# Performance work log

Hardware: AMD Instinct MI355X
Metric: run time of the kernel (lower is better)

Reference implementation:

```python
import jax, jax.numpy as jnp
import numpy as np

G, N_AST = 8192, 32
D_EMB, H_IN, ENC, H_OUT = 128, 64, 128, 128
N_STMT, E_STMT, N_SEL = G, 32768, 4096
EPS, NEG = 1e-5, 0.2


def _bn(x, g, b):
    # PyG BatchNorm (BatchNorm1d over nodes), training-mode batch stats (biased var)
    mu = x.mean(0)
    var = ((x - mu) ** 2).mean(0)
    return (x - mu) * jax.lax.rsqrt(var + EPS) * g + b


def _seg_softmax(logits, seg, n):
    # numerically stable softmax over edges grouped by destination node
    m = jax.ops.segment_max(logits, seg, num_segments=n)
    m = jnp.where(jnp.isfinite(m), m, 0.0)
    e = jnp.exp(logits - m[seg])
    s = jax.ops.segment_sum(e, seg, num_segments=n)
    return e / jnp.maximum(s[seg], 1e-16)


def _gat(x, src, dst, emask, W, a_src, a_dst, bias, heads, C, n):
    # PyG GATConv: add self-loops, leaky_relu(0.2) attention, concat heads, + bias
    h = (x @ W).reshape(n, heads, C)
    asrc = (h * a_src).sum(-1)  # [n, H]
    adst = (h * a_dst).sum(-1)
    loops = jnp.arange(n, dtype=src.dtype)
    s = jnp.concatenate([src, loops])
    d = jnp.concatenate([dst, loops])
    m = jnp.concatenate([emask, jnp.ones(n, bool)])
    logits = jax.nn.leaky_relu(asrc[s] + adst[d], NEG)
    logits = jnp.where(m[:, None], logits, -1e9)
    alpha = _seg_softmax(logits, d, n)  # [E, H]
    msg = jnp.where(m[:, None, None], alpha[:, :, None] * h[s], 0.0)
    out = jax.ops.segment_sum(msg, d, num_segments=n)
    return out.reshape(n, heads * C) + bias


def _topk(x, src, dst, emask, w, n_per_g, ratio, num_g):
    # PyG TopKPooling: score = tanh(x.w/||w||), keep top ceil(ratio*n) per graph,
    # gate kept features by score, remap/filter edges (here: mask + remap).
    k = int(np.ceil(ratio * n_per_g))
    score = (x @ w) / jnp.linalg.norm(w)  # [num_g*n_per_g]
    top_sc, top_idx = jax.lax.top_k(score.reshape(num_g, n_per_g), k)
    perm = (top_idx + jnp.arange(num_g)[:, None] * n_per_g).reshape(-1)
    new_x = x[perm] * jnp.tanh(top_sc).reshape(-1, 1)
    new_id = jnp.full((num_g * n_per_g,), -1, jnp.int32).at[perm].set(
        jnp.arange(num_g * k, dtype=jnp.int32))
    ns, nd = new_id[src], new_id[dst]
    valid = emask & (ns >= 0) & (nd >= 0)
    return new_x, jnp.maximum(ns, 0), jnp.maximum(nd, 0), valid, k


def _rgat(x, src, dst, etype, W, q, katt, bias, heads, C, n):
    # PyG RGATConv: per-relation weight, additive self-attention, across-relation softmax
    h0, h1 = x @ W[0], x @ W[1]  # [n, H*C]
    rel = (etype == 1)[:, None]
    out_j = jnp.where(rel, h1[src], h0[src])
    out_i = jnp.where(rel, h1[dst], h0[dst])
    logits = jax.nn.leaky_relu(out_i @ q + out_j @ katt, NEG)  # [E, H]
    alpha = _seg_softmax(logits, dst, n)
    msg = alpha[:, :, None] * out_j.reshape(-1, heads, C)
    out = jax.ops.segment_sum(msg, dst, num_segments=n)
    return out.reshape(n, heads * C) + bias


def setup_inputs() -> dict:
    key = jax.random.key(0)
    ks = jax.random.split(key, 20)
    rng = np.random.default_rng(0)
    # AST forest: random tree per statement graph (parent -> child edges)
    parents = np.stack([rng.integers(0, i, size=G) for i in range(1, N_AST)], axis=1)
    offs = (np.arange(G) * N_AST)[:, None]
    ast_src = jnp.asarray((parents + offs).reshape(-1), jnp.int32)
    ast_dst = jnp.asarray((np.broadcast_to(np.arange(1, N_AST), (G, N_AST - 1)) + offs).reshape(-1), jnp.int32)
    # statement-level graph; edge_type sorted (relation 0 block then relation 1)
    stmt_src = jnp.asarray(rng.integers(0, N_STMT, E_STMT), jnp.int32)
    stmt_dst = jnp.asarray(rng.integers(0, N_STMT, E_STMT), jnp.int32)
    stmt_etype = jnp.asarray(np.sort(rng.integers(0, 2, E_STMT)), jnp.int32)
    sel_index = jnp.asarray(np.sort(rng.choice(N_STMT, N_SEL, replace=False)), jnp.int32)

    def nrm(k, shape, s=0.1):
        return jax.random.normal(k, shape, jnp.float32) * s

    return dict(
        ast_x=jax.random.normal(ks[0], (G * N_AST, D_EMB), jnp.float32),
        ast_src=ast_src, ast_dst=ast_dst,
        stmt_src=stmt_src, stmt_dst=stmt_dst, stmt_etype=stmt_etype,
        sel_index=sel_index,
        gat0_W=nrm(ks[1], (D_EMB, 3 * H_IN)),
        gat0_asrc=nrm(ks[2], (3, H_IN)), gat0_adst=nrm(ks[3], (3, H_IN)),
        gat0_b=jnp.zeros((3 * H_IN,), jnp.float32),
        bn0_g=jnp.ones((3 * H_IN,), jnp.float32), bn0_b=jnp.zeros((3 * H_IN,), jnp.float32),
        pool0_w=nrm(ks[4], (3 * H_IN,)),
        gat1_W=nrm(ks[5], (3 * H_IN, H_IN)),
        gat1_asrc=nrm(ks[6], (1, H_IN)), gat1_adst=nrm(ks[7], (1, H_IN)),
        gat1_b=jnp.zeros((H_IN,), jnp.float32),
        bn1_g=jnp.ones((H_IN,), jnp.float32), bn1_b=jnp.zeros((H_IN,), jnp.float32),
        pool1_w=nrm(ks[8], (H_IN,)),
        enc_w1=nrm(ks[9], (H_IN, H_IN)), enc_b1=jnp.zeros((H_IN,), jnp.float32),
        enc_w2=nrm(ks[10], (H_IN, ENC)), enc_b2=jnp.zeros((ENC,), jnp.float32),
        rgat0_W=nrm(ks[11], (2, ENC, 3 * H_OUT)),
        rgat0_q=nrm(ks[12], (3 * H_OUT, 3)), rgat0_k=nrm(ks[13], (3 * H_OUT, 3)),
        rgat0_b=jnp.zeros((3 * H_OUT,), jnp.float32),
        bnc0_g=jnp.ones((3 * H_OUT,), jnp.float32), bnc0_b=jnp.zeros((3 * H_OUT,), jnp.float32),
        rgat1_W=nrm(ks[14], (2, 3 * H_OUT, H_OUT)),
        rgat1_q=nrm(ks[15], (H_OUT, 1)), rgat1_k=nrm(ks[16], (H_OUT, 1)),
        rgat1_b=jnp.zeros((H_OUT,), jnp.float32),
        bnc1_g=jnp.ones((H_OUT,), jnp.float32), bnc1_b=jnp.zeros((H_OUT,), jnp.float32),
        clf_w1=nrm(ks[17], (H_OUT, H_OUT)), clf_b1=jnp.zeros((H_OUT,), jnp.float32),
        clf_w2=nrm(ks[18], (H_OUT, 1)), clf_b2=jnp.zeros((1,), jnp.float32),
    )


def reference(ast_x, ast_src, ast_dst, stmt_src, stmt_dst, stmt_etype, sel_index,
              gat0_W, gat0_asrc, gat0_adst, gat0_b, bn0_g, bn0_b, pool0_w,
              gat1_W, gat1_asrc, gat1_adst, gat1_b, bn1_g, bn1_b, pool1_w,
              enc_w1, enc_b1, enc_w2, enc_b2,
              rgat0_W, rgat0_q, rgat0_k, rgat0_b, bnc0_g, bnc0_b,
              rgat1_W, rgat1_q, rgat1_k, rgat1_b, bnc1_g, bnc1_b,
              clf_w1, clf_b1, clf_w2, clf_b2):
    # ---- StatementEncoder over batch of AST graphs ----
    N0 = G * N_AST
    m_full = jnp.ones(ast_src.shape[0], bool)
    h = _gat(ast_x, ast_src, ast_dst, m_full, gat0_W, gat0_asrc, gat0_adst, gat0_b, 3, H_IN, N0)
    h = _bn(jnp.tanh(h), bn0_g, bn0_b)
    h, s, d, m, k0 = _topk(h, ast_src, ast_dst, m_full, pool0_w, N_AST, 0.7, G)
    h = jax.nn.relu(h)
    h = _gat(h, s, d, m, gat1_W, gat1_asrc, gat1_adst, gat1_b, 1, H_IN, G * k0)
    h = _bn(jnp.tanh(h), bn1_g, bn1_b)
    h, s, d, m, k1 = _topk(h, s, d, m, pool1_w, k0, 0.5, G)
    h = jax.nn.relu(h.reshape(G, k1, H_IN).max(axis=1))  # global_max_pool then relu
    x = jax.nn.relu(h @ enc_w1 + enc_b1) @ enc_w2 + enc_b2  # [G, ENC]
    # ---- StatementClassifier over statement graph ----
    h = _rgat(x, stmt_src, stmt_dst, stmt_etype, rgat0_W, rgat0_q, rgat0_k, rgat0_b, 3, H_OUT, N_STMT)
    h = _bn(jnp.tanh(h), bnc0_g, bnc0_b)
    h = _rgat(h, stmt_src, stmt_dst, stmt_etype, rgat1_W, rgat1_q, rgat1_k, rgat1_b, 1, H_OUT, N_STMT)
    h = _bn(jnp.tanh(h), bnc1_g, bnc1_b)
    h = h[sel_index]  # index_select(idx2index(idx))
    return jax.nn.sigmoid(jax.nn.relu(h @ clf_w1 + clf_b1) @ clf_w2 + clf_b2)
```

## Files before the change

kernel.cpp:

```cpp
#include <hip/hip_runtime.h>
#include <cstddef>
#include <cstdint>

constexpr int G      = 8192;
constexpr int NAST   = 32;
constexpr int N0     = G * NAST;
constexpr int D_EMB  = 128;
constexpr int C0     = 192;
constexpr int H_IN   = 64;
constexpr int K0     = 23;
constexpr int N1     = G * K0;
constexpr int K1     = 12;
constexpr int ENC    = 128;
constexpr int NSTMT  = 8192;
constexpr int EST    = 32768;
constexpr int HO3    = 384;
constexpr int HOUT   = 128;
constexpr int NSEL   = 4096;

__global__ __launch_bounds__(256) void fused_gat0(
    const float* __restrict__ X, const float* __restrict__ W,
    const int* __restrict__ ast_src,
    const float* __restrict__ asrc_w, const float* __restrict__ adst_w,
    const float* __restrict__ bias,
    float* __restrict__ out, float* __restrict__ psum, float* __restrict__ psq)
{
    __shared__ char smem[52736];
    int tid = threadIdx.x;
    int b = blockIdx.x;
    int row0 = b * 64;

    float* As = (float*)smem;
    float* Bs = As + 32 * 65;

    int ra = tid >> 3;
    int c0 = (tid & 7) * 24;
    int lr = tid >> 2;
    int lk = (tid & 3) * 8;
    int bkk = tid >> 3;
    int bc0 = (tid & 7) * 24;

    float acc0[24] = {};
    float acc1[24] = {};

    for (int kt = 0; kt < 128; kt += 32) {
        const float* ap = X + (size_t)(row0 + lr) * 128 + kt + lk;
        float4 a0 = *(const float4*)ap;
        float4 a1 = *(const float4*)(ap + 4);
        As[(lk + 0) * 65 + lr] = a0.x; As[(lk + 1) * 65 + lr] = a0.y;
        As[(lk + 2) * 65 + lr] = a0.z; As[(lk + 3) * 65 + lr] = a0.w;
        As[(lk + 4) * 65 + lr] = a1.x; As[(lk + 5) * 65 + lr] = a1.y;
        As[(lk + 6) * 65 + lr] = a1.z; As[(lk + 7) * 65 + lr] = a1.w;
        const float* bp = W + (size_t)(kt + bkk) * 192 + bc0;
        #pragma unroll
        for (int u = 0; u < 6; ++u)
            *(float4*)&Bs[bkk * 200 + bc0 + u * 4] = *(const float4*)(bp + u * 4);
        __syncthreads();
        #pragma unroll
        for (int kk = 0; kk < 32; ++kk) {
            float a0v = As[kk * 65 + ra];
            float a1v = As[kk * 65 + 32 + ra];
            const float* bb = &Bs[kk * 200 + c0];
            #pragma unroll
            for (int u = 0; u < 6; ++u) {
                float4 b4 = *(const float4*)(bb + u * 4);
                acc0[u * 4 + 0] += a0v * b4.x; acc1[u * 4 + 0] += a1v * b4.x;
                acc0[u * 4 + 1] += a0v * b4.y; acc1[u * 4 + 1] += a1v * b4.y;
                acc0[u * 4 + 2] += a0v * b4.z; acc1[u * 4 + 2] += a1v * b4.z;
                acc0[u * 4 + 3] += a0v * b4.w; acc1[u * 4 + 3] += a1v * b4.w;
            }
        }
        __syncthreads();
    }

    float* Cs  = (float*)smem;
    float* as_ = Cs + 64 * 193;
    float* ad_ = as_ + 192;
    float* aS  = ad_ + 192;
    float* aP  = aS + 192;
    int*  parl = (int*)(aP + 192);

    #pragma unroll
    for (int u = 0; u < 24; ++u) {
        Cs[ra * 193 + c0 + u]        = acc0[u];
        Cs[(ra + 32) * 193 + c0 + u] = acc1[u];
    }
    if (tid < 62) {
        int q = tid / 31, j = tid % 31 + 1;
        int g = 2 * b + q;
        parl[q * 32 + j] = ast_src[(size_t)g * 31 + j - 1] - g * 32 + q * 32;
    }
    if (tid < 2) parl[tid * 32] = -1;
    __syncthreads();

    for (int task = tid; task < 384; task += 256) {
        int r = task / 6, q6 = task % 6, hh = q6 >> 1, sd = q6 & 1;
        const float* w = (sd ? adst_w : asrc_w) + hh * 64;
        const float* crow = &Cs[r * 193 + hh * 64];
        float s = 0.f;
        for (int c = 0; c < 64; ++c) s += crow[c] * w[c];
        (sd ? ad_ : as_)[r * 3 + hh] = s;
    }
    __syncthreads();
    if (tid < 192) {
        int r = tid / 3, hh = tid % 3, p = parl[r];
        if (p < 0) { aS[r * 3 + hh] = 1.f; aP[r * 3 + hh] = 0.f; }
        else {
            float ls = as_[r * 3 + hh] + ad_[r * 3 + hh]; ls = ls > 0 ? ls : 0.2f * ls;
            float lp = as_[p * 3 + hh] + ad_[r * 3 + hh]; lp = lp > 0 ? lp : 0.2f * lp;
            float m = fmaxf(ls, lp);
            float es = __expf(ls - m) , ep = __expf(lp - m);
            es = expf(ls - m); ep = expf(lp - m);
            float inv = 1.f / (es + ep);
            aS[r * 3 + hh] = es * inv; aP[r * 3 + hh] = ep * inv;
        }
    }
    __syncthreads();
    if (tid < 192) {
        int j = tid, hh = j >> 6;
        float bj = bias[j];
        float s = 0.f, s2 = 0.f;
        for (int r = 0; r < 64; ++r) {
            int p = parl[r];
            float v = aS[r * 3 + hh] * Cs[r * 193 + j];
            if (p >= 0) v += aP[r * 3 + hh] * Cs[p * 193 + j];
            v = tanhf(v + bj);
            out[(size_t)(row0 + r) * 192 + j] = v;
            s += v; s2 += v * v;
        }
        psum[(size_t)j * 4096 + b] = s;
        psq [(size_t)j * 4096 + b] = s2;
    }
}

__global__ __launch_bounds__(256) void bn_finalize(
    const float* __restrict__ psum, const float* __restrict__ psq, int nb, float R,
    const float* __restrict__ gamma, const float* __restrict__ beta,
    const float* __restrict__ w,
    float* __restrict__ ga, float* __restrict__ be,
    float* __restrict__ gw, float* __restrict__ bw)
{
    int j = blockIdx.x, t = threadIdx.x;
    const float* ps = psum + (size_t)j * nb;
    const float* pq = psq + (size_t)j * nb;
    float s = 0.f, s2 = 0.f;
    for (int i = t; i < nb; i += 256) { s += ps[i]; s2 += pq[i]; }
    __shared__ float r1[4], r2[4];
    for (int o = 32; o > 0; o >>= 1) { s += __shfl_down(s, o, 64); s2 += __shfl_down(s2, o, 64); }
    if ((t & 63) == 0) { r1[t >> 6] = s; r2[t >> 6] = s2; }
    __syncthreads();
    if (t == 0) {
        float S = r1[0] + r1[1] + r1[2] + r1[3];
        float S2 = r2[0] + r2[1] + r2[2] + r2[3];
        float mu = S / R, var = S2 / R - mu * mu;
        float inv = 1.f / sqrtf(var + 1e-5f);
        float gaj = gamma[j] * inv, bej = beta[j] - mu * gaj;
        ga[j] = gaj; be[j] = bej; gw[j] = gaj * w[j]; bw[j] = bej * w[j];
    }
}

__global__ __launch_bounds__(256) void score_topk0(
    const float* __restrict__ hA, const int* __restrict__ ast_src,
    const float* __restrict__ gw, const float* __restrict__ bw,
    const float* __restrict__ w,
    int* __restrict__ oldrow, float* __restrict__ gate23, int* __restrict__ parloc)
{
    __shared__ float swv[192];
    __shared__ float sc[32];
    __shared__ int nid[32];
    __shared__ float wparts[4], bparts[4];
    int g = blockIdx.x, t = threadIdx.x;
    if (t < 192) swv[t] = gw[t];
    float ws = (t < 192) ? w[t] * w[t] : 0.f;
    float bs = (t < 192) ? bw[t] : 0.f;
    for (int o = 32; o > 0; o >>= 1) { ws += __shfl_down(ws, o, 64); bs += __shfl_down(bs, o, 64); }
    if ((t & 63) == 0) { wparts[t >> 6] = ws; bparts[t >> 6] = bs; }
    __syncthreads();
    float invn = rsqrtf(wparts[0] + wparts[1] + wparts[2] + wparts[3]);
    invn = 1.f / sqrtf(1.f / (invn * invn));
    {
        float tot = wparts[0] + wparts[1] + wparts[2] + wparts[3];
        invn = 1.f / sqrtf(tot);
    }
    float sb = bparts[0] + bparts[1] + bparts[2] + bparts[3];

    int r = t >> 3, j0 = (t & 7) * 24;
    const float* row = hA + ((size_t)g * 32 + r) * 192 + j0;
    const float4* row4 = (const float4*)row;
    const float4* sw4 = (const float4*)(swv + j0);
    float s = 0.f;
    #pragma unroll
    for (int u = 0; u < 6; ++u) {
        float4 a = row4[u], bv = sw4[u];
        s += a.x * bv.x + a.y * bv.y + a.z * bv.z + a.w * bv.w;
    }
    for (int o = 4; o > 0; o >>= 1) s += __shfl_down(s, o, 8);
    if ((t & 7) == 0) sc[r] = (s + sb) * invn;
    __syncthreads();
    if (t < 32) {
        float v = sc[t]; int rank = 0;
        for (int j = 0; j < 32; ++j) rank += (sc[j] > v) || (sc[j] == v && j < t);
        nid[t] = (rank < 23) ? rank : -1;
    }
    __syncthreads();
    if (t < 32 && nid[t] >= 0) {
        int rank = nid[t];
        oldrow[g * 23 + rank] = g * 32 + t;
        gate23[g * 23 + rank] = tanhf(sc[t]);
        int pl = -1;
        if (t > 0) {
            int p = ast_src[(size_t)g * 31 + t - 1] - g * 32;
            pl = nid[p];
        }
        parloc[g * 23 + rank] = pl;
    }
}

__global__ __launch_bounds__(256) void gemm_gather(
    const float* __restrict__ A, const float* __restrict__ B, float* __restrict__ C,
    const int* __restrict__ rowmap, const float* __restrict__ gate,
    const float* __restrict__ ga, const float* __restrict__ be)
{
    __shared__ float As[16 * 68];
    __shared__ float Bs[16 * 68];
    __shared__ float gas[192], bes[192];
    int tid = threadIdx.x, bm = blockIdx.x;
    if (tid < 192) { gas[tid] = ga[tid]; bes[tid] = be[tid]; }
    int arow = tid >> 2, aks = (tid & 3) * 4;
    int brow = tid >> 4, bns = (tid & 15) * 4;
    int tm = tid >> 4, tn = tid & 15;
    float acc[4][4] = {};
    int grow = bm * 64 + arow;
    int old = rowmap[grow];
    float gt = gate[grow];
    const float* ap = A + (size_t)old * 192;
    __syncthreads();
    for (int kt = 0; kt < 192; kt += 16) {
        float4 av = *(const float4*)(ap + kt + aks);
        int kb = kt + aks;
        av.x = fmaxf((av.x * gas[kb + 0] + bes[kb + 0]) * gt, 0.f);
        av.y = fmaxf((av.y * gas[kb + 1] + bes[kb + 1]) * gt, 0.f);
        av.z = fmaxf((av.z * gas[kb + 2] + bes[kb + 2]) * gt, 0.f);
        av.w = fmaxf((av.w * gas[kb + 3] + bes[kb + 3]) * gt, 0.f);
        As[(aks + 0) * 68 + arow] = av.x;
        As[(aks + 1) * 68 + arow] = av.y;
        As[(aks + 2) * 68 + arow] = av.z;
        As[(aks + 3) * 68 + arow] = av.w;
        *(float4*)&Bs[brow * 68 + bns] = *(const float4*)(B + (size_t)(kt + brow) * 64 + bns);
        __syncthreads();
        #pragma unroll
        for (int kk = 0; kk < 16; ++kk) {
            float4 a4 = *(const float4*)&As[kk * 68 + (tm << 2)];
            float4 b4 = *(const float4*)&Bs[kk * 68 + (tn << 2)];
            float a_[4] = {a4.x, a4.y, a4.z, a4.w};
            float b_[4] = {b4.x, b4.y, b4.z, b4.w};
            #pragma unroll
            for (int i = 0; i < 4; ++i)
                #pragma unroll
                for (int j = 0; j < 4; ++j)
                    acc[i][j] += a_[i] * b_[j];
        }
        __syncthreads();
    }
    #pragma unroll
    for (int i = 0; i < 4; ++i) {
        int rr = bm * 64 + (tm << 2) + i;
        float4 o = {acc[i][0], acc[i][1], acc[i][2], acc[i][3]};
        *(float4*)(C + (size_t)rr * 64 + (tn << 2)) = o;
    }
}

__global__ __launch_bounds__(64) void gat1_att_bn(
    float* __restrict__ h, const int* __restrict__ parloc,
    const float* __restrict__ aw_s, const float* __restrict__ aw_d,
    const float* __restrict__ bias,
    float* __restrict__ psum, float* __restrict__ psq)
{
    __shared__ float hs[23 * 65];
    __shared__ float as_[23], ad_[23], aS[23], aP[23];
    __shared__ int parl[23];
    int g = blockIdx.x, t = threadIdx.x;
    float* base = h + (size_t)g * 23 * 64;
    for (int r = 0; r < 23; ++r) hs[r * 65 + t] = base[r * 64 + t];
    if (t < 23) parl[t] = parloc[g * 23 + t];
    __syncthreads();
    if (t < 46) {
        int r = t >> 1, sd = t & 1;
        const float* w = sd ? aw_d : aw_s;
        const float* row = &hs[r * 65];
        float s = 0.f;
        for (int c = 0; c < 64; ++c) s += row[c] * w[c];
        (sd ? ad_ : as_)[r] = s;
    }
    __syncthreads();
    if (t < 23) {
        int p = parl[t];
        if (p < 0) { aS[t] = 1.f; aP[t] = 0.f; }
        else {
            float ls = as_[t] + ad_[t]; ls = ls > 0 ? ls : 0.2f * ls;
            float lp = as_[p] + ad_[t]; lp = lp > 0 ? lp : 0.2f * lp;
            float m = fmaxf(ls, lp);
            float es = expf(ls - m), ep = expf(lp - m);
            float inv = 1.f / (es + ep);
            aS[t] = es * inv; aP[t] = ep * inv;
        }
    }
    __syncthreads();
    float bj = bias[t], s = 0.f, s2 = 0.f;
    for (int r = 0; r < 23; ++r) {
        int p = parl[r];
        float v = aS[r] * hs[r * 65 + t];
        if (p >= 0) v += aP[r] * hs[p * 65 + t];
        v = tanhf(v + bj);
        base[r * 64 + t] = v;
        s += v; s2 += v * v;
    }
    psum[(size_t)t * 8192 + g] = s;
    psq [(size_t)t * 8192 + g] = s2;
}

__global__ __launch_bounds__(128) void pool1_mlp(
    const float* __restrict__ h,
    const float* __restrict__ gw, const float* __restrict__ bw,
    const float* __restrict__ w,
    const float* __restrict__ ga, const float* __restrict__ be,
    const float* __restrict__ w1, const float* __restrict__ b1,
    const float* __restrict__ w2, const float* __restrict__ b2,
    float* __restrict__ xenc)
{
    __shared__ float hs[23 * 65];
    __shared__ float sc[23];
    __shared__ int keep[23];
    __shared__ float feat[64], t1[64];
    __shared__ float consts[2];
    int g = blockIdx.x, t = threadIdx.x;
    const float* base = h + (size_t)g * 23 * 64;
    {
        int c = t & 63;
        for (int r = t >> 6; r < 23; r += 2) hs[r * 65 + c] = base[r * 64 + c];
    }
    if (t < 64) {
        float ws = w[t] * w[t], bs = bw[t];
        for (int o = 32; o > 0; o >>= 1) { ws += __shfl_down(ws, o, 64); bs += __shfl_down(bs, o, 64); }
        if (t == 0) { consts[0] = 1.f / sqrtf(ws); consts[1] = bs; }
    }
    __syncthreads();
    if (t < 23) {
        const float* row = &hs[t * 65];
        float s = 0.f;
        for (int c = 0; c < 64; ++c) s += row[c] * gw[c];
        sc[t] = (s + consts[1]) * consts[0];
    }
    __syncthreads();
    if (t < 23) {
        float v = sc[t]; int rank = 0;
        for (int j = 0; j < 23; ++j) rank += (sc[j] > v) || (sc[j] == v && j < t);
        keep[t] = rank < 12;
    }
    __syncthreads();
    if (t < 23) sc[t] = tanhf(sc[t]);
    __syncthreads();
    if (t < 64) {
        float m = -1e30f, gac = ga[t], bec = be[t];
        for (int r = 0; r < 23; ++r)
            if (keep[r]) m = fmaxf(m, (hs[r * 65 + t] * gac + bec) * sc[r]);
        feat[t] = fmaxf(m, 0.f);
    }
    __syncthreads();
    if (t < 64) {
        float acc = b1[t];
        for (int c = 0; c < 64; ++c) acc += feat[c] * w1[c * 64 + t];
        t1[t] = fmaxf(acc, 0.f);
    }
    __syncthreads();
    float acc = b2[t];
    for (int j = 0; j < 64; ++j) acc += t1[j] * w2[j * 128 + t];
    xenc[(size_t)g * 128 + t] = acc;
}

__global__ __launch_bounds__(256) void gemm_nn(
    const float* __restrict__ A, const float* __restrict__ B, float* __restrict__ C,
    int M, int N, int K)
{
    __shared__ float As[16 * 68];
    __shared__ float Bs[16 * 68];
    int tid = threadIdx.x;
    int bm = blockIdx.x, bn = blockIdx.y;
    int arow = tid >> 2, aks = (tid & 3) * 4;
    int brow = tid >> 4, bns = (tid & 15) * 4;
    int tm = tid >> 4, tn = tid & 15;
    float acc[4][4] = {};
    const float* ap = A + (size_t)(bm * 64 + arow) * K;
    for (int kt = 0; kt < K; kt += 16) {
        float4 av = *(const float4*)(ap + kt + aks);
        As[(aks + 0) * 68 + arow] = av.x;
        As[(aks + 1) * 68 + arow] = av.y;
        As[(aks + 2) * 68 + arow] = av.z;
        As[(aks + 3) * 68 + arow] = av.w;
        *(float4*)&Bs[brow * 68 + bns] = *(const float4*)(B + (size_t)(kt + brow) * N + bn * 64 + bns);
        __syncthreads();
        #pragma unroll
        for (int kk = 0; kk < 16; ++kk) {
            float4 a4 = *(const float4*)&As[kk * 68 + (tm << 2)];
            float4 b4 = *(const float4*)&Bs[kk * 68 + (tn << 2)];
            float a_[4] = {a4.x, a4.y, a4.z, a4.w};
            float b_[4] = {b4.x, b4.y, b4.z, b4.w};
            #pragma unroll
            for (int i = 0; i < 4; ++i)
                #pragma unroll
                for (int j = 0; j < 4; ++j)
                    acc[i][j] += a_[i] * b_[j];
        }
        __syncthreads();
    }
    #pragma unroll
    for (int i = 0; i < 4; ++i) {
        int r = bm * 64 + (tm << 2) + i;
        float4 o = {acc[i][0], acc[i][1], acc[i][2], acc[i][3]};
        *(float4*)(C + (size_t)r * N + bn * 64 + (tn << 2)) = o;
    }
}

__global__ void bn_stats(const float* __restrict__ X, int R,
                         float* __restrict__ sum, float* __restrict__ sumsq)
{
    int t = threadIdx.x;
    int C = blockDim.x;
    float s = 0.f, s2 = 0.f;
    for (int r = blockIdx.x; r < R; r += gridDim.x) {
        float v = X[(size_t)r * C + t];
        s += v; s2 += v * v;
    }
    atomicAdd(&sum[t], s);
    atomicAdd(&sumsq[t], s2);
}

__global__ void bn_apply(float* __restrict__ X, int R,
                         const float* __restrict__ sum, const float* __restrict__ sumsq,
                         const float* __restrict__ gam, const float* __restrict__ bet)
{
    int t = threadIdx.x;
    int C = blockDim.x;
    float invR = 1.f / (float)R;
    float mu = sum[t] * invR;
    float var = sumsq[t] * invR - mu * mu;
    float inv = 1.f / sqrtf(var + 1e-5f);
    float ga = gam[t] * inv;
    float be = bet[t] - mu * ga;
    for (int r = blockIdx.x; r < R; r += gridDim.x) {
        size_t idx = (size_t)r * C + t;
        X[idx] = X[idx] * ga + be;
    }
}

__global__ __launch_bounds__(256) void rgat_qk3(
    const float* __restrict__ h0, const float* __restrict__ h1,
    const float* __restrict__ q, const float* __restrict__ k,
    float* __restrict__ qi, float* __restrict__ kj)
{
    int n = blockIdx.x, t = threadIdx.x;
    float p[12] = {};
    for (int d = t; d < HO3; d += 256) {
        float v0 = h0[(size_t)n * HO3 + d], v1 = h1[(size_t)n * HO3 + d];
        #pragma unroll
        for (int hh = 0; hh < 3; ++hh) {
            float qw = q[d * 3 + hh], kw = k[d * 3 + hh];
            p[hh]     += v0 * qw;  p[3 + hh] += v0 * kw;
            p[6 + hh] += v1 * qw;  p[9 + hh] += v1 * kw;
        }
    }
    __shared__ float red[4][12];
    #pragma unroll
    for (int i = 0; i < 12; ++i) {
        float x = p[i];
        for (int o = 32; o > 0; o >>= 1) x += __shfl_down(x, o, 64);
        if ((t & 63) == 0) red[t >> 6][i] = x;
    }
    __syncthreads();
    if (t < 12) {
        float s = red[0][t] + red[1][t] + red[2][t] + red[3][t];
        int rel = t / 6, rem = t % 6, isk = rem / 3, hh = rem % 3;
        float* dst = isk ? kj : qi;
        dst[((size_t)rel * NSTMT + n) * 3 + hh] = s;
    }
}

__global__ void edge_logits3(const int* __restrict__ src, const int* __restrict__ dst,
                             const int* __restrict__ et,
                             const float* __restrict__ qi, const float* __restrict__ kj,
                             float* __restrict__ logits)
{
    int e = blockIdx.x * 256 + threadIdx.x;
    if (e >= EST) return;
    int r = et[e], s = src[e], d = dst[e];
    #pragma unroll
    for (int hh = 0; hh < 3; ++hh) {
        float x = qi[((size_t)r * NSTMT + d) * 3 + hh] + kj[((size_t)r * NSTMT + s) * 3 + hh];
        logits[e * 3 + hh] = x > 0 ? x : 0.2f * x;
    }
}

__global__ void count_deg(const int* __restrict__ dst, int* __restrict__ deg)
{
    int e = blockIdx.x * 256 + threadIdx.x;
    if (e < EST) atomicAdd(&deg[dst[e]], 1);
}

__global__ void scan_deg(const int* __restrict__ deg, int* __restrict__ offa)
{
    __shared__ int ts[1024];
    int t = threadIdx.x;
    int base = t * 8;
    int loc[8]; int s = 0;
    #pragma unroll
    for (int i = 0; i < 8; ++i) { loc[i] = s; s += deg[base + i]; }
    ts[t] = s;
    __syncthreads();
    for (int o = 1; o < 1024; o <<= 1) {
        int v = (t >= o) ? ts[t - o] : 0;
        __syncthreads();
        ts[t] += v;
        __syncthreads();
    }
    int prev = (t == 0) ? 0 : ts[t - 1];
    #pragma unroll
    for (int i = 0; i < 8; ++i) offa[base + i] = prev + loc[i];
    if (t == 1023) offa[8192] = ts[1023];
}

__global__ void scatter_csr(const int* __restrict__ dst, const int* __restrict__ offa,
                            int* __restrict__ cnt, int* __restrict__ csr)
{
    int e = blockIdx.x * 256 + threadIdx.x;
    if (e < EST) {
        int d = dst[e];
        int pos = offa[d] + atomicAdd(&cnt[d], 1);
        csr[pos] = e;
    }
}

__global__ __launch_bounds__(256) void rgat_agg3(
    const float* __restrict__ h0, const float* __restrict__ h1,
    const int* __restrict__ offa, const int* __restrict__ csr,
    const int* __restrict__ src, const int* __restrict__ et,
    const float* __restrict__ logits, const float* __restrict__ bias,
    float* __restrict__ out)
{
    int n = blockIdx.x, t = threadIdx.x;
    int o0 = offa[n], deg = offa[n + 1] - o0;
    __shared__ float m[3], sden[3];
    __shared__ float al[64][3];
    __shared__ int esrc[64], erel[64];
    if (t < 3) {
        float mm = -1e30f;
        for (int i = 0; i < deg; ++i) mm = fmaxf(mm, logits[csr[o0 + i] * 3 + t]);
        float ss = 0.f;
        for (int i = 0; i < deg; ++i) ss += expf(logits[csr[o0 + i] * 3 + t] - mm);
        m[t] = mm; sden[t] = fmaxf(ss, 1e-16f);
    }
    __syncthreads();
    float acc0 = 0.f, acc1 = 0.f;
    for (int c0 = 0; c0 < deg; c0 += 64) {
        int cn = min(64, deg - c0);
        if (t < cn) { int e = csr[o0 + c0 + t]; esrc[t] = src[e]; erel[t] = et[e]; }
        if (t < cn * 3) {
            int ee = t / 3, hh = t % 3;
            int e = csr[o0 + c0 + ee];
            al[ee][hh] = expf(logits[e * 3 + hh] - m[hh]) / sden[hh];
        }
        __syncthreads();
        for (int i = 0; i < cn; ++i) {
            const float* hb = (erel[i] ? h1 : h0) + (size_t)esrc[i] * HO3;
            acc0 += al[i][t >> 7] * hb[t];
            if (t < 128) acc1 += al[i][(t + 256) >> 7] * hb[t + 256];
        }
        __syncthreads();
    }
    out[(size_t)n * HO3 + t] = tanhf(acc0 + bias[t]);
    if (t < 128) out[(size_t)n * HO3 + t + 256] = tanhf(acc1 + bias[t + 256]);
}

__global__ __launch_bounds__(128) void rgat_qk1(
    const float* __restrict__ h0, const float* __restrict__ h1,
    const float* __restrict__ q, const float* __restrict__ k,
    float* __restrict__ qi, float* __restrict__ kj)
{
    int n = blockIdx.x, t = threadIdx.x;
    float v0 = h0[(size_t)n * 128 + t], v1 = h1[(size_t)n * 128 + t];
    float p0 = v0 * q[t], p1 = v0 * k[t], p2 = v1 * q[t], p3 = v1 * k[t];
    __shared__ float red[2][4];
    for (int o = 32; o > 0; o >>= 1) {
        p0 += __shfl_down(p0, o, 64); p1 += __shfl_down(p1, o, 64);
        p2 += __shfl_down(p2, o, 64); p3 += __shfl_down(p3, o, 64);
    }
    if ((t & 63) == 0) { int w = t >> 6; red[w][0] = p0; red[w][1] = p1; red[w][2] = p2; red[w][3] = p3; }
    __syncthreads();
    if (t < 4) {
        float s = red[0][t] + red[1][t];
        if (t == 0) qi[n] = s;
        else if (t == 1) kj[n] = s;
        else if (t == 2) qi[NSTMT + n] = s;
        else kj[NSTMT + n] = s;
    }
}

__global__ void edge_logits1(const int* __restrict__ src, const int* __restrict__ dst,
                             const int* __restrict__ et,
                             const float* __restrict__ qi, const float* __restrict__ kj,
                             float* __restrict__ logits)
{
    int e = blockIdx.x * 256 + threadIdx.x;
    if (e >= EST) return;
    int r = et[e], s = src[e], d = dst[e];
    float x = qi[(size_t)r * NSTMT + d] + kj[(size_t)r * NSTMT + s];
    logits[e] = x > 0 ? x : 0.2f * x;
}

__global__ __launch_bounds__(128) void rgat_agg1(
    const float* __restrict__ h0, const float* __restrict__ h1,
    const int* __restrict__ offa, const int* __restrict__ csr,
    const int* __restrict__ src, const int* __restrict__ et,
    const float* __restrict__ logits, const float* __restrict__ bias,
    float* __restrict__ out)
{
    int n = blockIdx.x, t = threadIdx.x;
    int o0 = offa[n], deg = offa[n + 1] - o0;
    __shared__ float m1, s1;
    __shared__ float al[64];
    __shared__ int esrc[64], erel[64];
    if (t == 0) {
        float mm = -1e30f;
        for (int i = 0; i < deg; ++i) mm = fmaxf(mm, logits[csr[o0 + i]]);
        float ss = 0.f;
        for (int i = 0; i < deg; ++i) ss += expf(logits[csr[o0 + i]] - mm);
        m1 = mm; s1 = fmaxf(ss, 1e-16f);
    }
    __syncthreads();
    float acc = 0.f;
    for (int c0 = 0; c0 < deg; c0 += 64) {
        int cn = min(64, deg - c0);
        if (t < cn) {
            int e = csr[o0 + c0 + t];
            esrc[t] = src[e]; erel[t] = et[e];
            al[t] = expf(logits[e] - m1) / s1;
        }
        __syncthreads();
        for (int i = 0; i < cn; ++i)
            acc += al[i] * ((erel[i] ? h1 : h0)[(size_t)esrc[i] * 128 + t]);
        __syncthreads();
    }
    out[(size_t)n * 128 + t] = tanhf(acc + bias[t]);
}

__global__ __launch_bounds__(128) void classifier(
    const float* __restrict__ x, const int* __restrict__ sel,
    const float* __restrict__ w1, const float* __restrict__ b1,
    const float* __restrict__ w2, const float* __restrict__ b2,
    float* __restrict__ out)
{
    __shared__ float row[128];
    __shared__ float t1[128];
    __shared__ float red[2];
    int b = blockIdx.x, t = threadIdx.x;
    int n = sel[b];
    row[t] = x[(size_t)n * 128 + t];
    __syncthreads();
    float acc = b1[t];
    for (int k = 0; k < 128; ++k) acc += row[k] * w1[k * 128 + t];
    t1[t] = fmaxf(acc, 0.f);
    __syncthreads();
    float p = t1[t] * w2[t];
    for (int o = 32; o > 0; o >>= 1) p += __shfl_down(p, o, 64);
    if ((t & 63) == 0) red[t >> 6] = p;
    __syncthreads();
    if (t == 0) {
        float z = red[0] + red[1] + b2[0];
        out[b] = 1.f / (1.f + expf(-z));
    }
}

constexpr size_t OFF_HA     = 0;
constexpr size_t OFF_BN0    = 201326592;
constexpr size_t OFF_BN1    = OFF_BN0 + 3072;
constexpr size_t OFF_OLDROW = OFF_BN1 + 1024;
constexpr size_t OFF_GATE   = OFF_OLDROW + 753664;
constexpr size_t OFF_PARLOC = OFF_GATE + 753664;
constexpr size_t OFF_HB     = OFF_PARLOC + 753664;
constexpr size_t OFF_XENC   = OFF_HB + 48234496;
constexpr size_t OFF_BNSUM  = OFF_XENC + 4194304;
constexpr size_t OFF_BNSQ   = OFF_BNSUM + 1536;
constexpr size_t WS_NEEDED  = OFF_BNSQ + 1536;
constexpr size_t OFF_H0R  = 0;
constexpr size_t OFF_H1R  = 12582912;
constexpr size_t OFF_OUT0 = 25165824;
constexpr size_t OFF_G0   = 37748736;
constexpr size_t OFF_G1   = 41943040;
constexpr size_t OFF_OUT1 = 46137344;
constexpr size_t OFF_QI3  = 50331648;
constexpr size_t OFF_KJ3  = 50528256;
constexpr size_t OFF_LG3  = 50724864;
constexpr size_t OFF_QI1  = 51118080;
constexpr size_t OFF_KJ1  = 51183616;
constexpr size_t OFF_LG1  = 51249152;
constexpr size_t OFF_DEG  = 51380224;
constexpr size_t OFF_OFFA = 51412992;
constexpr size_t OFF_CNT  = 51446016;
constexpr size_t OFF_CSR  = 51478784;

extern "C" void kernel_launch(void* const* d_in, const int* in_sizes, int n_in,
                              void* d_out, int out_size, void* d_ws, size_t ws_size,
                              hipStream_t stream)
{
    if (n_in < 41 || ws_size < WS_NEEDED) return;

    const float* ast_x    = (const float*)d_in[0];
    const int*   ast_src  = (const int*)d_in[1];
    const int*   stmt_src = (const int*)d_in[3];
    const int*   stmt_dst = (const int*)d_in[4];
    const int*   stmt_et  = (const int*)d_in[5];
    const int*   sel      = (const int*)d_in[6];
    const float* gat0_W    = (const float*)d_in[7];
    const float* gat0_asrc = (const float*)d_in[8];
    const float* gat0_adst = (const float*)d_in[9];
    const float* gat0_b    = (const float*)d_in[10];
    const float* bn0_g     = (const float*)d_in[11];
    const float* bn0_b     = (const float*)d_in[12];
    const float* pool0_w   = (const float*)d_in[13];
    const float* gat1_W    = (const float*)d_in[14];
    const float* gat1_asrc = (const float*)d_in[15];
    const float* gat1_adst = (const float*)d_in[16];
    const float* gat1_b    = (const float*)d_in[17];
    const float* bn1_g     = (const float*)d_in[18];
    const float* bn1_b     = (const float*)d_in[19];
    const float* pool1_w   = (const float*)d_in[20];
    const float* enc_w1    = (const float*)d_in[21];
    const float* enc_b1    = (const float*)d_in[22];
    const float* enc_w2    = (const float*)d_in[23];
    const float* enc_b2    = (const float*)d_in[24];
    const float* rgat0_W   = (const float*)d_in[25];
    const float* rgat0_q   = (const float*)d_in[26];
    const float* rgat0_k   = (const float*)d_in[27];
    const float* rgat0_b   = (const float*)d_in[28];
    const float* bnc0_g    = (const float*)d_in[29];
    const float* bnc0_b    = (const float*)d_in[30];
    const float* rgat1_W   = (const float*)d_in[31];
    const float* rgat1_q   = (const float*)d_in[32];
    const float* rgat1_k   = (const float*)d_in[33];
    const float* rgat1_b   = (const float*)d_in[34];
    const float* bnc1_g    = (const float*)d_in[35];
    const float* bnc1_b    = (const float*)d_in[36];
    const float* clf_w1    = (const float*)d_in[37];
    const float* clf_b1    = (const float*)d_in[38];
    const float* clf_w2    = (const float*)d_in[39];
    const float* clf_b2    = (const float*)d_in[40];

    char* ws = (char*)d_ws;
    float* hA     = (float*)(ws + OFF_HA);
    float* ga0    = (float*)(ws + OFF_BN0);
    float* be0    = ga0 + 192;
    float* gw0    = be0 + 192;
    float* bw0    = gw0 + 192;
    float* ga1    = (float*)(ws + OFF_BN1);
    float* be1    = ga1 + 64;
    float* gw1    = be1 + 64;
    float* bw1    = gw1 + 64;
    int*   oldrow = (int*)(ws + OFF_OLDROW);
    float* gate23 = (float*)(ws + OFF_GATE);
    int*   parloc = (int*)(ws + OFF_PARLOC);
    float* hB     = (float*)(ws + OFF_HB);
    float* psum0  = (float*)(ws + OFF_HB);
    float* psq0   = psum0 + 192 * 4096;
    float* xenc   = (float*)(ws + OFF_XENC);
    float* psum1  = (float*)(ws + OFF_XENC);
    float* psq1   = psum1 + 64 * 8192;
    float* bnsum  = (float*)(ws + OFF_BNSUM);
    float* bnsq   = (float*)(ws + OFF_BNSQ);

    float* h0r  = (float*)(ws + OFF_H0R);
    float* h1r  = (float*)(ws + OFF_H1R);
    float* out0 = (float*)(ws + OFF_OUT0);
    float* g0   = (float*)(ws + OFF_G0);
    float* g1   = (float*)(ws + OFF_G1);
    float* out1 = (float*)(ws + OFF_OUT1);
    float* qi3  = (float*)(ws + OFF_QI3);
    float* kj3  = (float*)(ws + OFF_KJ3);
    float* lg3  = (float*)(ws + OFF_LG3);
    float* qi1  = (float*)(ws + OFF_QI1);
    float* kj1  = (float*)(ws + OFF_KJ1);
    float* lg1  = (float*)(ws + OFF_LG1);
    int*   deg  = (int*)(ws + OFF_DEG);
    int*   offa = (int*)(ws + OFF_OFFA);
    int*   cnt  = (int*)(ws + OFF_CNT);
    int*   csr  = (int*)(ws + OFF_CSR);

    fused_gat0<<<4096, 256, 0, stream>>>(ast_x, gat0_W, ast_src, gat0_asrc, gat0_adst,
                                         gat0_b, hA, psum0, psq0);
    bn_finalize<<<192, 256, 0, stream>>>(psum0, psq0, 4096, (float)N0,
                                         bn0_g, bn0_b, pool0_w, ga0, be0, gw0, bw0);
    score_topk0<<<G, 256, 0, stream>>>(hA, ast_src, gw0, bw0, pool0_w,
                                       oldrow, gate23, parloc);
    gemm_gather<<<N1 / 64, 256, 0, stream>>>(hA, gat1_W, hB, oldrow, gate23, ga0, be0);
    gat1_att_bn<<<G, 64, 0, stream>>>(hB, parloc, gat1_asrc, gat1_adst, gat1_b,
                                      psum1, psq1);
    bn_finalize<<<64, 256, 0, stream>>>(psum1, psq1, 8192, (float)N1,
                                        bn1_g, bn1_b, pool1_w, ga1, be1, gw1, bw1);
    pool1_mlp<<<G, 128, 0, stream>>>(hB, gw1, bw1, pool1_w, ga1, be1,
                                     enc_w1, enc_b1, enc_w2, enc_b2, xenc);

    gemm_nn<<<dim3(NSTMT / 64, HO3 / 64), 256, 0, stream>>>(xenc, rgat0_W, h0r, NSTMT, HO3, ENC);
    gemm_nn<<<dim3(NSTMT / 64, HO3 / 64), 256, 0, stream>>>(xenc, rgat0_W + (size_t)ENC * HO3, h1r, NSTMT, HO3, ENC);
    rgat_qk3<<<NSTMT, 256, 0, stream>>>(h0r, h1r, rgat0_q, rgat0_k, qi3, kj3);
    edge_logits3<<<EST / 256, 256, 0, stream>>>(stmt_src, stmt_dst, stmt_et, qi3, kj3, lg3);
    hipMemsetAsync(deg, 0, 32768, stream);
    hipMemsetAsync(cnt, 0, 32768, stream);
    count_deg<<<EST / 256, 256, 0, stream>>>(stmt_dst, deg);
    scan_deg<<<1, 1024, 0, stream>>>(deg, offa);
    scatter_csr<<<EST / 256, 256, 0, stream>>>(stmt_dst, offa, cnt, csr);
    rgat_agg3<<<NSTMT, 256, 0, stream>>>(h0r, h1r, offa, csr, stmt_src, stmt_et, lg3, rgat0_b, out0);
    hipMemsetAsync(bnsum, 0, 3072, stream);
    bn_stats<<<256, HO3, 0, stream>>>(out0, NSTMT, bnsum, bnsq);
    bn_apply<<<256, HO3, 0, stream>>>(out0, NSTMT, bnsum, bnsq, bnc0_g, bnc0_b);
    gemm_nn<<<dim3(NSTMT / 64, HOUT / 64), 256, 0, stream>>>(out0, rgat1_W, g0, NSTMT, HOUT, HO3);
    gemm_nn<<<dim3(NSTMT / 64, HOUT / 64), 256, 0, stream>>>(out0, rgat1_W + (size_t)HO3 * HOUT, g1, NSTMT, HOUT, HO3);
    rgat_qk1<<<NSTMT, 128, 0, stream>>>(g0, g1, rgat1_q, rgat1_k, qi1, kj1);
    edge_logits1<<<EST / 256, 256, 0, stream>>>(stmt_src, stmt_dst, stmt_et, qi1, kj1, lg1);
    rgat_agg1<<<NSTMT, 128, 0, stream>>>(g0, g1, offa, csr, stmt_src, stmt_et, lg1, rgat1_b, out1);
    hipMemsetAsync(bnsum, 0, 3072, stream);
    bn_stats<<<256, HOUT, 0, stream>>>(out1, NSTMT, bnsum, bnsq);
    bn_apply<<<256, HOUT, 0, stream>>>(out1, NSTMT, bnsum, bnsq, bnc1_g, bnc1_b);
    classifier<<<NSEL, 128, 0, stream>>>(out1, sel, clf_w1, clf_b1, clf_w2, clf_b2, (float*)d_out);
}
```

Baseline: 984.6 us.

## Retile gat0 GEMM to 8x8 register blocks and transpose BN partial-sum layout

Rewrites the first GAT GEMM to use 192 threads, each computing an 8x8 output tile from float4 shared-memory loads, in place of a 2x24 tile per thread. The goal is more arithmetic per shared-memory load and vectorized stores of the C tile. The BN partial-sum layout also changes from feature-major to block-major, so the per-block writes are coalesced, and bn_finalize now reads them strided. Some dead redundant math in score_topk0 and the GAT softmax is removed as well. Risks are higher register pressure from 64 accumulators and strided reads in the finalize kernel.

```diff
diff --git a/kernel.cpp b/kernel.cpp
--- a/kernel.cpp
+++ b/kernel.cpp
@@ -18,72 +18,66 @@
 constexpr int HOUT   = 128;
 constexpr int NSEL   = 4096;
 
-__global__ __launch_bounds__(256) void fused_gat0(
+__global__ __launch_bounds__(192) void fused_gat0(
     const float* __restrict__ X, const float* __restrict__ W,
     const int* __restrict__ ast_src,
     const float* __restrict__ asrc_w, const float* __restrict__ adst_w,
     const float* __restrict__ bias,
     float* __restrict__ out, float* __restrict__ psum, float* __restrict__ psq)
 {
-    __shared__ char smem[52736];
+    __shared__ float smem[13376];
+    float* As = smem;
+    float* Bs = smem + 2176;
     int tid = threadIdx.x;
     int b = blockIdx.x;
     int row0 = b * 64;
-
-    float* As = (float*)smem;
-    float* Bs = As + 32 * 65;
-
-    int ra = tid >> 3;
-    int c0 = (tid & 7) * 24;
-    int lr = tid >> 2;
-    int lk = (tid & 3) * 8;
-    int bkk = tid >> 3;
-    int bc0 = (tid & 7) * 24;
-
-    float acc0[24] = {};
-    float acc1[24] = {};
+    int tm = tid / 24;
+    int tn = tid % 24;
+
+    float acc[8][8] = {};
 
     for (int kt = 0; kt < 128; kt += 32) {
-        const float* ap = X + (size_t)(row0 + lr) * 128 + kt + lk;
-        float4 a0 = *(const float4*)ap;
-        float4 a1 = *(const float4*)(ap + 4);
-        As[(lk + 0) * 65 + lr] = a0.x; As[(lk + 1) * 65 + lr] = a0.y;
-        As[(lk + 2) * 65 + lr] = a0.z; As[(lk + 3) * 65 + lr] = a0.w;
-        As[(lk + 4) * 65 + lr] = a1.x; As[(lk + 5) * 65 + lr] = a1.y;
-        As[(lk + 6) * 65 + lr] = a1.z; As[(lk + 7) * 65 + lr] = a1.w;
-        const float* bp = W + (size_t)(kt + bkk) * 192 + bc0;
-        #pragma unroll
-        for (int u = 0; u < 6; ++u)
-            *(float4*)&Bs[bkk * 200 + bc0 + u * 4] = *(const float4*)(bp + u * 4);
-        __syncthreads();
-        #pragma unroll
+        for (int i = tid; i < 512; i += 192) {
+            int r = i & 63, q = i >> 6;
+            float4 v = *(const float4*)(X + (size_t)(row0 + r) * 128 + kt + q * 4);
+            As[(q * 4 + 0) * 68 + r] = v.x;
+            As[(q * 4 + 1) * 68 + r] = v.y;
+            As[(q * 4 + 2) * 68 + r] = v.z;
+            As[(q * 4 + 3) * 68 + r] = v.w;
+        }
+        for (int i = tid; i < 1536; i += 192) {
+            int k = i / 48, c4 = (i % 48) * 4;
+            *(float4*)&Bs[k * 200 + c4] = *(const float4*)(W + (size_t)(kt + k) * 192 + c4);
+        }
+        __syncthreads();
+        #pragma unroll 4
         for (int kk = 0; kk < 32; ++kk) {
-            float a0v = As[kk * 65 + ra];
-            float a1v = As[kk * 65 + 32 + ra];
-            const float* bb = &Bs[kk * 200 + c0];
+            float4 a0 = *(const float4*)&As[kk * 68 + tm * 8];
+            float4 a1 = *(const float4*)&As[kk * 68 + tm * 8 + 4];
+            float4 b0 = *(const float4*)&Bs[kk * 200 + tn * 8];
+            float4 b1 = *(const float4*)&Bs[kk * 200 + tn * 8 + 4];
+            float a_[8] = {a0.x, a0.y, a0.z, a0.w, a1.x, a1.y, a1.z, a1.w};
+            float b_[8] = {b0.x, b0.y, b0.z, b0.w, b1.x, b1.y, b1.z, b1.w};
             #pragma unroll
-            for (int u = 0; u < 6; ++u) {
-                float4 b4 = *(const float4*)(bb + u * 4);
-                acc0[u * 4 + 0] += a0v * b4.x; acc1[u * 4 + 0] += a1v * b4.x;
-                acc0[u * 4 + 1] += a0v * b4.y; acc1[u * 4 + 1] += a1v * b4.y;
-                acc0[u * 4 + 2] += a0v * b4.z; acc1[u * 4 + 2] += a1v * b4.z;
-                acc0[u * 4 + 3] += a0v * b4.w; acc1[u * 4 + 3] += a1v * b4.w;
-            }
-        }
-        __syncthreads();
-    }
-
-    float* Cs  = (float*)smem;
-    float* as_ = Cs + 64 * 193;
+            for (int i = 0; i < 8; ++i)
+                #pragma unroll
+                for (int j = 0; j < 8; ++j)
+                    acc[i][j] += a_[i] * b_[j];
+        }
+        __syncthreads();
+    }
+
+    float* Cs  = smem;
+    float* as_ = smem + 12544;
     float* ad_ = as_ + 192;
     float* aS  = ad_ + 192;
     float* aP  = aS + 192;
     int*  parl = (int*)(aP + 192);
 
     #pragma unroll
-    for (int u = 0; u < 24; ++u) {
-        Cs[ra * 193 + c0 + u]        = acc0[u];
-        Cs[(ra + 32) * 193 + c0 + u] = acc1[u];
+    for (int i = 0; i < 8; ++i) {
+        *(float4*)&Cs[(tm * 8 + i) * 196 + tn * 8]     = *(float4*)&acc[i][0];
+        *(float4*)&Cs[(tm * 8 + i) * 196 + tn * 8 + 4] = *(float4*)&acc[i][4];
     }
     if (tid < 62) {
         int q = tid / 31, j = tid % 31 + 1;
@@ -93,10 +87,10 @@
     if (tid < 2) parl[tid * 32] = -1;
     __syncthreads();
 
-    for (int task = tid; task < 384; task += 256) {
+    for (int task = tid; task < 384; task += 192) {
         int r = task / 6, q6 = task % 6, hh = q6 >> 1, sd = q6 & 1;
         const float* w = (sd ? adst_w : asrc_w) + hh * 64;
-        const float* crow = &Cs[r * 193 + hh * 64];
+        const float* crow = &Cs[r * 196 + hh * 64];
         float s = 0.f;
         for (int c = 0; c < 64; ++c) s += crow[c] * w[c];
         (sd ? ad_ : as_)[r * 3 + hh] = s;
@@ -109,42 +103,42 @@
             float ls = as_[r * 3 + hh] + ad_[r * 3 + hh]; ls = ls > 0 ? ls : 0.2f * ls;
             float lp = as_[p * 3 + hh] + ad_[r * 3 + hh]; lp = lp > 0 ? lp : 0.2f * lp;
             float m = fmaxf(ls, lp);
-            float es = __expf(ls - m) , ep = __expf(lp - m);
-            es = expf(ls - m); ep = expf(lp - m);
+            float es = expf(ls - m), ep = expf(lp - m);
             float inv = 1.f / (es + ep);
             aS[r * 3 + hh] = es * inv; aP[r * 3 + hh] = ep * inv;
         }
     }
     __syncthreads();
-    if (tid < 192) {
+    {
         int j = tid, hh = j >> 6;
         float bj = bias[j];
         float s = 0.f, s2 = 0.f;
         for (int r = 0; r < 64; ++r) {
             int p = parl[r];
-            float v = aS[r * 3 + hh] * Cs[r * 193 + j];
-            if (p >= 0) v += aP[r * 3 + hh] * Cs[p * 193 + j];
+            float v = aS[r * 3 + hh] * Cs[r * 196 + j];
+            if (p >= 0) v += aP[r * 3 + hh] * Cs[p * 196 + j];
             v = tanhf(v + bj);
             out[(size_t)(row0 + r) * 192 + j] = v;
             s += v; s2 += v * v;
         }
-        psum[(size_t)j * 4096 + b] = s;
-        psq [(size_t)j * 4096 + b] = s2;
+        psum[(size_t)b * 192 + j] = s;
+        psq [(size_t)b * 192 + j] = s2;
     }
 }
 
 __global__ __launch_bounds__(256) void bn_finalize(
-    const float* __restrict__ psum, const float* __restrict__ psq, int nb, float R,
+    const float* __restrict__ psum, const float* __restrict__ psq, int nb, int C, float R,
     const float* __restrict__ gamma, const float* __restrict__ beta,
     const float* __restrict__ w,
     float* __restrict__ ga, float* __restrict__ be,
     float* __restrict__ gw, float* __restrict__ bw)
 {
     int j = blockIdx.x, t = threadIdx.x;
-    const float* ps = psum + (size_t)j * nb;
-    const float* pq = psq + (size_t)j * nb;
     float s = 0.f, s2 = 0.f;
-    for (int i = t; i < nb; i += 256) { s += ps[i]; s2 += pq[i]; }
+    for (int i = t; i < nb; i += 256) {
+        s  += psum[(size_t)i * C + j];
+        s2 += psq [(size_t)i * C + j];
+    }
     __shared__ float r1[4], r2[4];
     for (int o = 32; o > 0; o >>= 1) { s += __shfl_down(s, o, 64); s2 += __shfl_down(s2, o, 64); }
     if ((t & 63) == 0) { r1[t >> 6] = s; r2[t >> 6] = s2; }
@@ -176,17 +170,11 @@
     for (int o = 32; o > 0; o >>= 1) { ws += __shfl_down(ws, o, 64); bs += __shfl_down(bs, o, 64); }
     if ((t & 63) == 0) { wparts[t >> 6] = ws; bparts[t >> 6] = bs; }
     __syncthreads();
-    float invn = rsqrtf(wparts[0] + wparts[1] + wparts[2] + wparts[3]);
-    invn = 1.f / sqrtf(1.f / (invn * invn));
-    {
-        float tot = wparts[0] + wparts[1] + wparts[2] + wparts[3];
-        invn = 1.f / sqrtf(tot);
-    }
+    float invn = 1.f / sqrtf(wparts[0] + wparts[1] + wparts[2] + wparts[3]);
     float sb = bparts[0] + bparts[1] + bparts[2] + bparts[3];
 
     int r = t >> 3, j0 = (t & 7) * 24;
-    const float* row = hA + ((size_t)g * 32 + r) * 192 + j0;
-    const float4* row4 = (const float4*)row;
+    const float4* row4 = (const float4*)(hA + ((size_t)g * 32 + r) * 192 + j0);
     const float4* sw4 = (const float4*)(swv + j0);
     float s = 0.f;
     #pragma unroll
@@ -315,8 +303,8 @@
         base[r * 64 + t] = v;
         s += v; s2 += v * v;
     }
-    psum[(size_t)t * 8192 + g] = s;
-    psq [(size_t)t * 8192 + g] = s2;
+    psum[(size_t)g * 64 + t] = s;
+    psq [(size_t)g * 64 + t] = s2;
 }
 
 __global__ __launch_bounds__(128) void pool1_mlp(
@@ -793,16 +781,16 @@
     int*   cnt  = (int*)(ws + OFF_CNT);
     int*   csr  = (int*)(ws + OFF_CSR);
 
-    fused_gat0<<<4096, 256, 0, stream>>>(ast_x, gat0_W, ast_src, gat0_asrc, gat0_adst,
+    fused_gat0<<<4096, 192, 0, stream>>>(ast_x, gat0_W, ast_src, gat0_asrc, gat0_adst,
                                          gat0_b, hA, psum0, psq0);
-    bn_finalize<<<192, 256, 0, stream>>>(psum0, psq0, 4096, (float)N0,
+    bn_finalize<<<192, 256, 0, stream>>>(psum0, psq0, 4096, 192, (float)N0,
                                          bn0_g, bn0_b, pool0_w, ga0, be0, gw0, bw0);
     score_topk0<<<G, 256, 0, stream>>>(hA, ast_src, gw0, bw0, pool0_w,
                                        oldrow, gate23, parloc);
     gemm_gather<<<N1 / 64, 256, 0, stream>>>(hA, gat1_W, hB, oldrow, gate23, ga0, be0);
     gat1_att_bn<<<G, 64, 0, stream>>>(hB, parloc, gat1_asrc, gat1_adst, gat1_b,
                                       psum1, psq1);
-    bn_finalize<<<64, 256, 0, stream>>>(psum1, psq1, 8192, (float)N1,
+    bn_finalize<<<64, 256, 0, stream>>>(psum1, psq1, 8192, 64, (float)N1,
                                         bn1_g, bn1_b, pool1_w, ga1, be1, gw1, bw1);
     pool1_mlp<<<G, 128, 0, stream>>>(hB, gw1, bw1, pool1_w, ga1, be1,
                                      enc_w1, enc_b1, enc_w2, enc_b2, xenc);
```

New measurement: 931.8 us. 1.06x faster.
